# Kernel optimization log

Measured on AMD Instinct MI355X. Metric: run time of the kernel, lower is better.

The kernel has to match this reference:

```python
import jax, jax.numpy as jnp
import numpy as np
from jax.scipy.ndimage import map_coordinates


def setup_inputs() -> dict:
    key = jax.random.key(0)
    k1, k2 = jax.random.split(key)
    B, C, H, W = 8, 4, 1024, 1024
    image = jax.random.normal(k1, (B, C, H, W), dtype=jnp.float32)
    # flow in pixels; scale a bit so displacements span several pixels
    flow = jax.random.normal(k2, (B, 2, H, W), dtype=jnp.float32) * 4.0
    return {"image": image, "flow": flow}


def _warp(image, flow):
    # image: [B, C, H, W], flow: [B, 2, H, W] (x-disp at channel 0, y-disp at channel 1)
    B, C, H, W = image.shape
    dt = flow.dtype
    xx = jnp.arange(W, dtype=dt)[None, None, :]   # [1,1,W]
    yy = jnp.arange(H, dtype=dt)[None, :, None]   # [1,H,1]
    vx = xx + flow[:, 0]                           # [B,H,W] absolute x coordinate
    vy = yy + flow[:, 1]                           # [B,H,W] absolute y coordinate
    # Source normalizes with the align_corners=True formula...
    gx = 2.0 * vx / max(W - 1, 1) - 1.0
    gy = 2.0 * vy / max(H - 1, 1) - 1.0
    # ...but samples with align_corners=False: unnormalize accordingly.
    ix = ((gx + 1.0) * W - 1.0) * 0.5
    iy = ((gy + 1.0) * H - 1.0) * 0.5
    # padding_mode='border': clamp source coordinates into the valid range.
    ix = jnp.clip(ix, 0.0, W - 1)
    iy = jnp.clip(iy, 0.0, H - 1)

    def sample_plane(img2d, iy_b, ix_b):
        # bilinear gather; mode='nearest' clamps indices (matches border padding)
        return map_coordinates(img2d, [iy_b, ix_b], order=1, mode='nearest')

    # vmap over batch, then over channels (coords shared across channels)
    per_batch = lambda img, iy_b, ix_b: jax.vmap(lambda c: sample_plane(c, iy_b, ix_b))(img)
    return jax.vmap(per_batch)(image, iy, ix)  # [B,C,H,W]


def reference(image, flow):
    return _warp(image, flow)
```

## Files before the change

kernel.cpp:

```cpp
#include <hip/hip_runtime.h>


#define BB 8
#define CC 4
#define HH 1024
#define WW 1024
#define HW (HH * WW)

typedef _Float16 h4 __attribute__((ext_vector_type(4)));
typedef _Float16 h8 __attribute__((ext_vector_type(8)));

__global__ __launch_bounds__(256) void interleave_fp16_kernel(
    const float* __restrict__ image,
    h4* __restrict__ ws)
{
    int idx = blockIdx.x * blockDim.x + threadIdx.x;
    int b = idx >> 20;
    int p = idx & (HW - 1);
    const float* base = image + (size_t)b * CC * HW + p;
    h4 v;
    v.x = (_Float16)base[0];
    v.y = (_Float16)base[HW];
    v.z = (_Float16)base[2 * HW];
    v.w = (_Float16)base[3 * HW];
    ws[idx] = v;
}

__global__ __launch_bounds__(256) void advect_gather_fp16_kernel(
    const _Float16* __restrict__ ws,
    const float* __restrict__ flow,
    float* __restrict__ out)
{
    int tx = threadIdx.x & 31;
    int ty = threadIdx.x >> 5;
    int x = (blockIdx.x << 5) + tx;
    int y = (blockIdx.y << 3) + ty;
    int b = blockIdx.z;

    const float* fl = flow + (size_t)b * 2 * HW + (size_t)y * WW + x;
    float fx = fl[0];
    float fy = fl[HW];

    const float sx = (float)WW / (float)(WW - 1);
    const float sy = (float)HH / (float)(HH - 1);

    float ix = ((float)x + fx) * sx - 0.5f;
    float iy = ((float)y + fy) * sy - 0.5f;
    ix = fminf(fmaxf(ix, 0.0f), (float)(WW - 1));
    iy = fminf(fmaxf(iy, 0.0f), (float)(HH - 1));

    int xl = min((int)ix, WW - 2);
    int yl = min((int)iy, HH - 2);
    float wx = ix - (float)xl;
    float wy = iy - (float)yl;

    const _Float16* wsb = ws + (size_t)b * HW * 4;
    const _Float16* p0 = wsb + ((size_t)yl * WW + xl) * 4;
    const _Float16* p1 = p0 + (size_t)WW * 4;

    h8 t0, t1;
    __builtin_memcpy(&t0, p0, 16);
    __builtin_memcpy(&t1, p1, 16);

    float u0 = 1.0f - wx;
    float v0 = 1.0f - wy;

    float* outb = out + (size_t)b * CC * HW + (size_t)y * WW + x;
#pragma unroll
    for (int c = 0; c < CC; ++c) {
        float top = u0 * (float)t0[c] + wx * (float)t0[4 + c];
        float bot = u0 * (float)t1[c] + wx * (float)t1[4 + c];
        outb[(size_t)c * HW] = v0 * top + wy * bot;
    }
}

__global__ __launch_bounds__(256) void advect_fallback_kernel(
    const float* __restrict__ image,
    const float* __restrict__ flow,
    float* __restrict__ out)
{
    int idx = blockIdx.x * blockDim.x + threadIdx.x;
    int x = idx & (WW - 1);
    int y = (idx >> 10) & (HH - 1);
    int b = idx >> 20;

    const float* fl = flow + (size_t)b * 2 * HW + (size_t)y * WW + x;
    float fx = fl[0];
    float fy = fl[HW];

    const float sx = (float)WW / (float)(WW - 1);
    const float sy = (float)HH / (float)(HH - 1);

    float ix = ((float)x + fx) * sx - 0.5f;
    float iy = ((float)y + fy) * sy - 0.5f;
    ix = fminf(fmaxf(ix, 0.0f), (float)(WW - 1));
    iy = fminf(fmaxf(iy, 0.0f), (float)(HH - 1));

    int xl = min((int)ix, WW - 2);
    int yl = min((int)iy, HH - 2);
    float wx = ix - (float)xl;
    float wy = iy - (float)yl;

    float w00 = (1.0f - wy) * (1.0f - wx);
    float w01 = (1.0f - wy) * wx;
    float w10 = wy * (1.0f - wx);
    float w11 = wy * wx;

    int o00 = yl * WW + xl;
    int o01 = o00 + 1;
    int o10 = o00 + WW;
    int o11 = o10 + 1;

    const float* imgb = image + (size_t)b * CC * HW;
    float* outb = out + (size_t)b * CC * HW;
    int op = y * WW + x;

#pragma unroll
    for (int c = 0; c < CC; ++c) {
        const float* p = imgb + (size_t)c * HW;
        float v = w00 * p[o00] + w01 * p[o01] + w10 * p[o10] + w11 * p[o11];
        outb[(size_t)c * HW + op] = v;
    }
}

extern "C" void kernel_launch(void* const* d_in, const int* in_sizes, int n_in,
                              void* d_out, int out_size, void* d_ws, size_t ws_size,
                              hipStream_t stream) {
    const float* image = (const float*)d_in[0];
    const float* flow  = (const float*)d_in[1];
    float* out = (float*)d_out;

    const size_t need = (size_t)BB * HW * CC * sizeof(_Float16);
    if (ws_size >= need) {
        const int total = BB * HH * WW;
        interleave_fp16_kernel<<<total / 256, 256, 0, stream>>>(image, (h4*)d_ws);
        dim3 grid(WW / 32, HH / 8, BB);
        advect_gather_fp16_kernel<<<grid, 256, 0, stream>>>((const _Float16*)d_ws, flow, out);
    } else {
        const int total = BB * HH * WW;
        advect_fallback_kernel<<<(total + 255) / 256, 256, 0, stream>>>(image, flow, out);
    }
}
```

Measured before the change: 309.4 us.

## Fuse fp16 interleave into warp kernel using LDS halo tile

Replaces the two-pass scheme (global fp16 interleaved workspace, then gather) with one kernel. Each block loads a 64x16 output tile plus a 16-pixel halo of all four channels into shared memory as interleaved fp16. It then does the bilinear gathers from LDS, falling back to fp32 global loads when a sample lands outside the halo. This removes the workspace write and re-read and one launch. In exchange it re-reads halo data across neighbouring blocks and adds a __syncthreads plus about 37KB of LDS per block, which may limit occupancy.

```diff
diff --git a/kernel.cpp b/kernel.cpp
--- a/kernel.cpp
+++ b/kernel.cpp
@@ -7,119 +7,120 @@
 #define WW 1024
 #define HW (HH * WW)
 
+#define TX 64
+#define TY 16
+#define HALO 16
+#define RW 98
+#define RH 49
+
 typedef _Float16 h4 __attribute__((ext_vector_type(4)));
 typedef _Float16 h8 __attribute__((ext_vector_type(8)));
 
-__global__ __launch_bounds__(256) void interleave_fp16_kernel(
-    const float* __restrict__ image,
-    h4* __restrict__ ws)
-{
-    int idx = blockIdx.x * blockDim.x + threadIdx.x;
-    int b = idx >> 20;
-    int p = idx & (HW - 1);
-    const float* base = image + (size_t)b * CC * HW + p;
-    h4 v;
-    v.x = (_Float16)base[0];
-    v.y = (_Float16)base[HW];
-    v.z = (_Float16)base[2 * HW];
-    v.w = (_Float16)base[3 * HW];
-    ws[idx] = v;
-}
-
-__global__ __launch_bounds__(256) void advect_gather_fp16_kernel(
-    const _Float16* __restrict__ ws,
-    const float* __restrict__ flow,
-    float* __restrict__ out)
-{
-    int tx = threadIdx.x & 31;
-    int ty = threadIdx.x >> 5;
-    int x = (blockIdx.x << 5) + tx;
-    int y = (blockIdx.y << 3) + ty;
-    int b = blockIdx.z;
-
-    const float* fl = flow + (size_t)b * 2 * HW + (size_t)y * WW + x;
-    float fx = fl[0];
-    float fy = fl[HW];
-
-    const float sx = (float)WW / (float)(WW - 1);
-    const float sy = (float)HH / (float)(HH - 1);
-
-    float ix = ((float)x + fx) * sx - 0.5f;
-    float iy = ((float)y + fy) * sy - 0.5f;
-    ix = fminf(fmaxf(ix, 0.0f), (float)(WW - 1));
-    iy = fminf(fmaxf(iy, 0.0f), (float)(HH - 1));
-
-    int xl = min((int)ix, WW - 2);
-    int yl = min((int)iy, HH - 2);
-    float wx = ix - (float)xl;
-    float wy = iy - (float)yl;
-
-    const _Float16* wsb = ws + (size_t)b * HW * 4;
-    const _Float16* p0 = wsb + ((size_t)yl * WW + xl) * 4;
-    const _Float16* p1 = p0 + (size_t)WW * 4;
-
-    h8 t0, t1;
-    __builtin_memcpy(&t0, p0, 16);
-    __builtin_memcpy(&t1, p1, 16);
-
-    float u0 = 1.0f - wx;
-    float v0 = 1.0f - wy;
-
-    float* outb = out + (size_t)b * CC * HW + (size_t)y * WW + x;
-#pragma unroll
-    for (int c = 0; c < CC; ++c) {
-        float top = u0 * (float)t0[c] + wx * (float)t0[4 + c];
-        float bot = u0 * (float)t1[c] + wx * (float)t1[4 + c];
-        outb[(size_t)c * HW] = v0 * top + wy * bot;
-    }
-}
-
-__global__ __launch_bounds__(256) void advect_fallback_kernel(
+__global__ __launch_bounds__(256) void advect_fused_kernel(
     const float* __restrict__ image,
     const float* __restrict__ flow,
     float* __restrict__ out)
 {
-    int idx = blockIdx.x * blockDim.x + threadIdx.x;
-    int x = idx & (WW - 1);
-    int y = (idx >> 10) & (HH - 1);
-    int b = idx >> 20;
+    __shared__ h4 lds[RH][RW];
 
-    const float* fl = flow + (size_t)b * 2 * HW + (size_t)y * WW + x;
-    float fx = fl[0];
-    float fy = fl[HW];
+    const int tid = threadIdx.x;
+    const int x0 = blockIdx.x * TX;
+    const int y0 = blockIdx.y * TY;
+    const int b  = blockIdx.z;
 
-    const float sx = (float)WW / (float)(WW - 1);
-    const float sy = (float)HH / (float)(HH - 1);
+    const float* img = image + (size_t)b * CC * HW;
 
-    float ix = ((float)x + fx) * sx - 0.5f;
-    float iy = ((float)y + fy) * sy - 0.5f;
-    ix = fminf(fmaxf(ix, 0.0f), (float)(WW - 1));
-    iy = fminf(fmaxf(iy, 0.0f), (float)(HH - 1));
+    for (int e = tid; e < RH * (RW / 2); e += 256) {
+        const int r  = e / (RW / 2);
+        const int pc = e - r * (RW / 2);
+        const int gy  = min(max(y0 - HALO + r, 0), HH - 1);
+        const int gxb = min(max(x0 - HALO + 2 * pc, 0), WW - 2);
+        const float* p = img + (size_t)gy * WW + gxb;
+        float2 c0, c1, c2, c3;
+        __builtin_memcpy(&c0, p,          8);
+        __builtin_memcpy(&c1, p + HW,     8);
+        __builtin_memcpy(&c2, p + 2 * HW, 8);
+        __builtin_memcpy(&c3, p + 3 * HW, 8);
+        h8 pr;
+        pr[0] = (_Float16)c0.x; pr[1] = (_Float16)c1.x;
+        pr[2] = (_Float16)c2.x; pr[3] = (_Float16)c3.x;
+        pr[4] = (_Float16)c0.y; pr[5] = (_Float16)c1.y;
+        pr[6] = (_Float16)c2.y; pr[7] = (_Float16)c3.y;
+        *(h8*)&lds[r][2 * pc] = pr;
+    }
+    __syncthreads();
 
-    int xl = min((int)ix, WW - 2);
-    int yl = min((int)iy, HH - 2);
-    float wx = ix - (float)xl;
-    float wy = iy - (float)yl;
+    const int tx = tid & 63;
+    const int x  = x0 + tx;
+    const int yb = y0 + ((tid >> 6) << 2);
 
-    float w00 = (1.0f - wy) * (1.0f - wx);
-    float w01 = (1.0f - wy) * wx;
-    float w10 = wy * (1.0f - wx);
-    float w11 = wy * wx;
+    const float sxs = (float)WW / (float)(WW - 1);
+    const float sys = (float)HH / (float)(HH - 1);
 
-    int o00 = yl * WW + xl;
-    int o01 = o00 + 1;
-    int o10 = o00 + WW;
-    int o11 = o10 + 1;
-
-    const float* imgb = image + (size_t)b * CC * HW;
+    const float* flb = flow + (size_t)b * 2 * HW;
     float* outb = out + (size_t)b * CC * HW;
-    int op = y * WW + x;
 
 #pragma unroll
-    for (int c = 0; c < CC; ++c) {
-        const float* p = imgb + (size_t)c * HW;
-        float v = w00 * p[o00] + w01 * p[o01] + w10 * p[o10] + w11 * p[o11];
-        outb[(size_t)c * HW + op] = v;
+    for (int k = 0; k < 4; ++k) {
+        const int y = yb + k;
+        const float* fl = flb + (size_t)y * WW + x;
+        const float fx = fl[0];
+        const float fy = fl[HW];
+
+        float ix = ((float)x + fx) * sxs - 0.5f;
+        float iy = ((float)y + fy) * sys - 0.5f;
+        ix = fminf(fmaxf(ix, 0.0f), (float)(WW - 1));
+        iy = fminf(fmaxf(iy, 0.0f), (float)(HH - 1));
+        const int xl = min((int)ix, WW - 2);
+        const int yl = min((int)iy, HH - 2);
+        const float wx = ix - (float)xl;
+        const float wy = iy - (float)yl;
+        const float u0 = 1.0f - wx;
+        const float v0 = 1.0f - wy;
+
+        const int rx = xl - x0 + HALO;
+        const int ry = yl - y0 + HALO;
+
+        float o0, o1, o2, o3;
+        if ((unsigned)rx <= (unsigned)(RW - 2) && (unsigned)ry <= (unsigned)(RH - 2)) {
+            const h4 a00 = lds[ry][rx];
+            const h4 a01 = lds[ry][rx + 1];
+            const h4 a10 = lds[ry + 1][rx];
+            const h4 a11 = lds[ry + 1][rx + 1];
+            o0 = v0 * (u0 * (float)a00[0] + wx * (float)a01[0])
+               + wy * (u0 * (float)a10[0] + wx * (float)a11[0]);
+            o1 = v0 * (u0 * (float)a00[1] + wx * (float)a01[1])
+               + wy * (u0 * (float)a10[1] + wx * (float)a11[1]);
+            o2 = v0 * (u0 * (float)a00[2] + wx * (float)a01[2])
+               + wy * (u0 * (float)a10[2] + wx * (float)a11[2]);
+            o3 = v0 * (u0 * (float)a00[3] + wx * (float)a01[3])
+               + wy * (u0 * (float)a10[3] + wx * (float)a11[3]);
+        } else {
+            const size_t o00 = (size_t)yl * WW + xl;
+            float2 t, bt;
+            const float* p0 = img + o00;
+            __builtin_memcpy(&t,  p0,      8);
+            __builtin_memcpy(&bt, p0 + WW, 8);
+            o0 = v0 * (u0 * t.x + wx * t.y) + wy * (u0 * bt.x + wx * bt.y);
+            p0 += HW;
+            __builtin_memcpy(&t,  p0,      8);
+            __builtin_memcpy(&bt, p0 + WW, 8);
+            o1 = v0 * (u0 * t.x + wx * t.y) + wy * (u0 * bt.x + wx * bt.y);
+            p0 += HW;
+            __builtin_memcpy(&t,  p0,      8);
+            __builtin_memcpy(&bt, p0 + WW, 8);
+            o2 = v0 * (u0 * t.x + wx * t.y) + wy * (u0 * bt.x + wx * bt.y);
+            p0 += HW;
+            __builtin_memcpy(&t,  p0,      8);
+            __builtin_memcpy(&bt, p0 + WW, 8);
+            o3 = v0 * (u0 * t.x + wx * t.y) + wy * (u0 * bt.x + wx * bt.y);
+        }
+
+        const size_t op = (size_t)y * WW + x;
+        outb[op]            = o0;
+        outb[HW + op]       = o1;
+        outb[2 * (size_t)HW + op] = o2;
+        outb[3 * (size_t)HW + op] = o3;
     }
 }
 
@@ -130,14 +131,6 @@
     const float* flow  = (const float*)d_in[1];
     float* out = (float*)d_out;
 
-    const size_t need = (size_t)BB * HW * CC * sizeof(_Float16);
-    if (ws_size >= need) {
-        const int total = BB * HH * WW;
-        interleave_fp16_kernel<<<total / 256, 256, 0, stream>>>(image, (h4*)d_ws);
-        dim3 grid(WW / 32, HH / 8, BB);
-        advect_gather_fp16_kernel<<<grid, 256, 0, stream>>>((const _Float16*)d_ws, flow, out);
-    } else {
-        const int total = BB * HH * WW;
-        advect_fallback_kernel<<<(total + 255) / 256, 256, 0, stream>>>(image, flow, out);
-    }
+    dim3 grid(WW / TX, HH / TY, BB);
+    advect_fused_kernel<<<grid, 256, 0, stream>>>(image, flow, out);
 }
```

Result: no change. 311.4 us (+0.6%).
